# Optimization experiments

Measured on AMD Instinct MI355X. Metric: run time of the kernel, lower is better.

## Reference

```python
import jax, jax.numpy as jnp
import numpy as np

K = 8192      # codebook_dim
D = 256       # embedding_dim
BETA = 0.25
DECAY = 0.99
EPS = 1e-05


def setup_inputs() -> dict:
    key = jax.random.key(0)
    k1, k2, k3, k4 = jax.random.split(key, 4)
    lim = 1.0 / K
    return {
        "z": jax.random.normal(k1, (8, D, 32, 32), dtype=jnp.float32),
        "embedding": jax.random.uniform(k2, (K, D), minval=-lim, maxval=lim, dtype=jnp.float32),
        "cluster_size": jax.random.uniform(k3, (K,), dtype=jnp.float32),
        "ema_w": jax.random.uniform(k4, (K, D), minval=-lim, maxval=lim, dtype=jnp.float32),
    }


def reference(z, embedding, cluster_size, ema_w):
    # z: [B, C, H, W] -> [B, H, W, C]
    zp = jnp.transpose(z, (0, 2, 3, 1))
    zf = zp.reshape(-1, D)                                  # [N, D]
    # squared L2 distance to each code: ||z||^2 + ||e||^2 - 2 z.e
    d = (jnp.sum(zf * zf, axis=1, keepdims=True)
         + jnp.sum(embedding * embedding, axis=1)
         - 2.0 * jnp.einsum("nd,kd->nk", zf, embedding))    # [N, K]
    idx = jnp.argmin(d, axis=1)                             # [N]
    z_q = embedding[idx].reshape(zp.shape)                  # [B, H, W, C]

    # EMA update (training branch), expressed with segment sums instead of
    # materializing the one-hot [N, K] matrix.
    counts = jax.ops.segment_sum(jnp.ones_like(idx, dtype=zf.dtype), idx, num_segments=K)
    new_cs = cluster_size * DECAY + (1.0 - DECAY) * counts
    n = jnp.sum(new_cs)
    new_cs = (new_cs + EPS) / (n + K * EPS) * n
    dw = jax.ops.segment_sum(zf, idx, num_segments=K)       # encodings.T @ zf
    new_ema_w = ema_w * DECAY + (1.0 - DECAY) * dw
    new_embedding = new_ema_w / new_cs[:, None]

    sg = jax.lax.stop_gradient
    loss = jnp.mean((sg(z_q) - zp) ** 2) + BETA * jnp.mean((z_q - sg(zp)) ** 2)
    # straight-through estimator, back to NCHW
    z_q_out = jnp.transpose(zp + sg(z_q - zp), (0, 3, 1, 2))
    return z_q_out, loss, idx, new_cs, new_ema_w, new_embedding
```

## Files before the change

kernel.cpp:

```cpp
#include <hip/hip_runtime.h>

#define CHW 262144
#define HWD 1024

typedef _Float16 v8h __attribute__((ext_vector_type(8)));
typedef _Float16 v4h __attribute__((ext_vector_type(4)));
typedef float    v4f __attribute__((ext_vector_type(4)));

static const unsigned OFF_ASQ  = 0;
static const unsigned OFF_BSQ  = 8192;
static const unsigned OFF_CNT  = 16384;
static const unsigned OFF_HEAD = 24576;
static const unsigned OFF_NXT  = 32768;
static const unsigned OFF_SCAL = 40960;
static const unsigned OFF_AH   = 40968;
static const unsigned OFF_AM   = 1089544;
static const unsigned OFF_BH   = 2138120;
static const unsigned OFF_BM   = 3186696;

#define GLL(g, l) __builtin_amdgcn_global_load_lds( \
    (const __attribute__((address_space(1))) void*)(g), \
    (__attribute__((address_space(3))) void*)(l), 16, 0, 0)

__global__ __launch_bounds__(256) void k_prep(const float* __restrict__ z,
        const float* __restrict__ emb, float* __restrict__ asq, float* __restrict__ bsq,
        _Float16* __restrict__ Bh, _Float16* __restrict__ Bm,
        _Float16* __restrict__ Ah, _Float16* __restrict__ Am,
        float* __restrict__ zerobase) {
    int bx = blockIdx.x;
    int t = threadIdx.x;
    if (bx < 32) {
        int n = bx * 256 + t;
        const float* p = z + (size_t)(n >> 10) * CHW + (n & 1023);
        float s = 0.f;
        #pragma unroll 8
        for (int c = 0; c < 256; ++c) { float v = p[(size_t)c << 10]; s = fmaf(v, v, s); }
        asq[n] = s;
    } else if (bx < 2080) {
        int w = (bx - 32) * 4 + (t >> 6);
        int lane = t & 63;
        float4 v = *(const float4*)(emb + (size_t)w * 256 + lane * 4);
        float s = v.x * v.x;
        s = fmaf(v.y, v.y, s); s = fmaf(v.z, v.z, s); s = fmaf(v.w, v.w, s);
        #pragma unroll
        for (int m = 1; m < 64; m <<= 1) s += __shfl_xor(s, m, 64);
        if (lane == 0) bsq[w] = s;
        float e0 = v.x * 8192.0f, e1 = v.y * 8192.0f, e2 = v.z * 8192.0f, e3 = v.w * 8192.0f;
        _Float16 h0 = (_Float16)e0, h1 = (_Float16)e1, h2 = (_Float16)e2, h3 = (_Float16)e3;
        v4h hv = {h0, h1, h2, h3};
        v4h mv = {(_Float16)(e0 - (float)h0),
                  (_Float16)(e1 - (float)h1),
                  (_Float16)(e2 - (float)h2),
                  (_Float16)(e3 - (float)h3)};
        *(v4h*)(Bh + (size_t)w * 256 + lane * 4) = hv;
        *(v4h*)(Bm + (size_t)w * 256 + lane * 4) = mv;
    } else if (bx < 2592) {
        __shared__ float s[64][65];
        int blk = bx - 2080;
        int hw0 = (blk & 15) * 64;
        int c0  = ((blk >> 4) & 3) * 64;
        int b   = blk >> 6;
        #pragma unroll
        for (int ii = 0; ii < 16; ++ii) {
            int e = t + ii * 256;
            int c = e >> 6, x = e & 63;
            s[c][x] = z[(size_t)b * CHW + (size_t)(c0 + c) * HWD + hw0 + x];
        }
        __syncthreads();
        int n2 = t >> 2, cq = (t & 3) * 16;
        _Float16 hbuf[16], mbuf[16];
        #pragma unroll
        for (int j = 0; j < 16; ++j) {
            float v = s[cq + j][n2];
            _Float16 h = (_Float16)v;
            float r = v - (float)h;
            hbuf[j] = h;
            mbuf[j] = (_Float16)r;
        }
        size_t off = ((size_t)b * 1024 + hw0 + n2) * 256 + c0 + cq;
        *(v8h*)(Ah + off)     = *(v8h*)(hbuf);
        *(v8h*)(Ah + off + 8) = *(v8h*)(hbuf + 8);
        *(v8h*)(Am + off)     = *(v8h*)(mbuf);
        *(v8h*)(Am + off + 8) = *(v8h*)(mbuf + 8);
    } else {
        int idx = (bx - 2592) * 1024 + t * 4;
        *(float4*)(zerobase + idx) = (float4){0.f, 0.f, 0.f, 0.f};
        if (bx == 2592 && t == 0)
            *(float4*)(zerobase + 24576) = (float4){0.f, 0.f, 0.f, 0.f};
    }
}

__global__ __launch_bounds__(512, 2) void k_main(
        const _Float16* __restrict__ Ah, const _Float16* __restrict__ Am,
        const _Float16* __restrict__ Bh, const _Float16* __restrict__ Bm,
        const float* __restrict__ asq, const float* __restrict__ bsq,
        unsigned* __restrict__ pdk) {
    __shared__ _Float16 lds[65536];
    const int bid = blockIdx.x;
    const int xcd = bid & 7, sblk = bid >> 3;
    const int kt = xcd * 4 + (sblk & 3);
    const int nt = sblk >> 2;
    const int n0 = nt * 256, k0 = kt * 256;
    const int t = threadIdx.x;
    const int lane = t & 63, w = t >> 6;
    const int wrow = w >> 1, wcol = w & 1;
    const int lm = lane & 15, quad = lane >> 4;

    v4f acc[4][8];
    #pragma unroll
    for (int i = 0; i < 4; ++i)
        #pragma unroll
        for (int j = 0; j < 8; ++j) acc[i][j] = (v4f){0.f,0.f,0.f,0.f};

    const int row0 = t >> 2;
    const int c40 = (t & 3) ^ ((row0 >> 1) & 3);
    const char* gA  = (const char*)Ah + (size_t)(n0 + row0) * 512 + c40 * 16;
    const char* gAm = (const char*)Am + (size_t)(n0 + row0) * 512 + c40 * 16;
    const char* gB  = (const char*)Bh + (size_t)(k0 + row0) * 512 + c40 * 16;
    const char* gBm = (const char*)Bm + (size_t)(k0 + row0) * 512 + c40 * 16;

    int sa[4], sb[8];
    #pragma unroll
    for (int i = 0; i < 4; ++i) {
        int mr = wrow * 64 + i * 16 + lm;
        sa[i] = mr * 32 + ((quad ^ ((mr >> 1) & 3)) * 8);
    }
    #pragma unroll
    for (int j = 0; j < 8; ++j) {
        int nr = wcol * 128 + j * 16 + lm;
        sb[j] = nr * 32 + ((quad ^ ((nr >> 1) & 3)) * 8);
    }

    auto stageA = [&](int s) {
        const size_t co = (size_t)s * 64;
        _Float16* l = lds + (s & 1) * 32768 + t * 8;
        GLL(gA + co,          l);
        GLL(gA + co + 65536,  l + 4096);
    };
    auto stageB = [&](int s) {
        const size_t co = (size_t)s * 64;
        _Float16* l = lds + (s & 1) * 32768 + t * 8;
        GLL(gB + co,          l + 16384);
        GLL(gB + co + 65536,  l + 20480);
    };
    auto stageM = [&](int s) {
        const size_t co = (size_t)s * 64;
        _Float16* l = lds + (s & 1) * 32768 + t * 8;
        GLL(gAm + co,         l + 8192);
        GLL(gAm + co + 65536, l + 12288);
        GLL(gBm + co,         l + 24576);
        GLL(gBm + co + 65536, l + 28672);
    };

#define MFMA16(A, B, C) __builtin_amdgcn_mfma_f32_16x16x32_f16(A, B, C, 0, 0, 0)

    stageA(0); stageB(0); stageM(0);
    asm volatile("s_waitcnt vmcnt(4)" ::: "memory");
    __builtin_amdgcn_s_barrier();

    #pragma unroll
    for (int s = 0; s < 8; ++s) {
        const _Float16* L = lds + (s & 1) * 32768;

        v8h fa[4], fb[8];
        #pragma unroll
        for (int i = 0; i < 4; ++i) fa[i] = *(const v8h*)(L + sa[i]);
        #pragma unroll
        for (int j = 0; j < 8; ++j) fb[j] = *(const v8h*)(L + 16384 + sb[j]);
        if (s < 7) stageA(s + 1);
        __builtin_amdgcn_sched_barrier(0);
        __builtin_amdgcn_s_barrier();
        asm volatile("s_waitcnt lgkmcnt(0)" ::: "memory");
        __builtin_amdgcn_sched_barrier(0);
        __builtin_amdgcn_s_setprio(1);
        #pragma unroll
        for (int j = 0; j < 8; ++j)
            #pragma unroll
            for (int i = 0; i < 4; ++i)
                acc[i][j] = MFMA16(fa[i], fb[j], acc[i][j]);
        __builtin_amdgcn_s_setprio(0);
        __builtin_amdgcn_sched_barrier(0);
        if (s < 7) { asm volatile("s_waitcnt vmcnt(2)" ::: "memory"); }
        else       { asm volatile("s_waitcnt vmcnt(0)" ::: "memory"); }
        __builtin_amdgcn_s_barrier();

        v8h fbm[8];
        #pragma unroll
        for (int j = 0; j < 8; ++j) fbm[j] = *(const v8h*)(L + 24576 + sb[j]);
        if (s < 7) stageB(s + 1);
        __builtin_amdgcn_sched_barrier(0);
        __builtin_amdgcn_s_barrier();
        asm volatile("s_waitcnt lgkmcnt(0)" ::: "memory");
        __builtin_amdgcn_sched_barrier(0);
        __builtin_amdgcn_s_setprio(1);
        #pragma unroll
        for (int j = 0; j < 8; ++j)
            #pragma unroll
            for (int i = 0; i < 4; ++i)
                acc[i][j] = MFMA16(fa[i], fbm[j], acc[i][j]);
        __builtin_amdgcn_s_setprio(0);
        __builtin_amdgcn_sched_barrier(0);
        __builtin_amdgcn_s_barrier();

        v8h fam[4], fb2[8];
        #pragma unroll
        for (int i = 0; i < 4; ++i) fam[i] = *(const v8h*)(L + 8192 + sa[i]);
        #pragma unroll
        for (int j = 0; j < 8; ++j) fb2[j] = *(const v8h*)(L + 16384 + sb[j]);
        if (s < 7) stageM(s + 1);
        __builtin_amdgcn_sched_barrier(0);
        __builtin_amdgcn_s_barrier();
        asm volatile("s_waitcnt lgkmcnt(0)" ::: "memory");
        __builtin_amdgcn_sched_barrier(0);
        __builtin_amdgcn_s_setprio(1);
        #pragma unroll
        for (int j = 0; j < 8; ++j)
            #pragma unroll
            for (int i = 0; i < 4; ++i)
                acc[i][j] = MFMA16(fam[i], fb2[j], acc[i][j]);
        __builtin_amdgcn_s_setprio(0);
        __builtin_amdgcn_sched_barrier(0);
        if (s < 7) { asm volatile("s_waitcnt vmcnt(4)" ::: "memory"); }
        else       { asm volatile("s_waitcnt vmcnt(0)" ::: "memory"); }
        __builtin_amdgcn_s_barrier();
    }
#undef MFMA16

    float bvv[8];
    #pragma unroll
    for (int j = 0; j < 8; ++j) bvv[j] = bsq[k0 + wcol * 128 + j * 16 + lm];
    __syncthreads();
    unsigned* lrow = (unsigned*)lds;
    #pragma unroll
    for (int i = 0; i < 4; ++i) {
        #pragma unroll
        for (int r = 0; r < 4; ++r) {
            int mm = wrow * 64 + i * 16 + quad * 4 + r;
            float av_ = asq[n0 + mm];
            #pragma unroll
            for (int jh = 0; jh < 2; ++jh) {
                unsigned best = 0xFFFFFFFFu;
                #pragma unroll
                for (int j4 = 0; j4 < 4; ++j4) {
                    const int j = jh * 4 + j4;
                    float S = acc[i][j][r] * 1.220703125e-4f;
                    float dd = (av_ + bvv[j]) - 2.0f * S;
                    float gv = dd - av_;
                    int mi = (int)(gv * 65536.0f) + 32768;
                    int col = k0 + wcol * 128 + j * 16 + lm;
                    unsigned key = ((unsigned)mi << 13) | (unsigned)col;
                    best = key < best ? key : best;
                }
                #pragma unroll
                for (int xm = 1; xm < 16; xm <<= 1) {
                    unsigned o = __shfl_xor(best, xm, 64);
                    best = o < best ? o : best;
                }
                if (lm == 0)
                    lrow[(mm >> 7) * 512 + (wcol * 2 + jh) * 128 + (mm & 127)] = best;
            }
        }
    }
    __syncthreads();
    #pragma unroll
    for (int u = 0; u < 2; ++u) {
        int e = t + u * 512;
        pdk[((size_t)(nt * 2 + (e >> 9)) * 128 + kt * 4 + ((e >> 7) & 3)) * 128 + (e & 127)]
            = lrow[e];
    }
}

__global__ __launch_bounds__(256) void k_zqr(const unsigned* __restrict__ pdk,
        const float* __restrict__ z, const float* __restrict__ emb, const float* __restrict__ cs,
        float* __restrict__ out_idx, int* __restrict__ cnt,
        int* __restrict__ head, int* __restrict__ nxt,
        float* __restrict__ out_zq, float* __restrict__ scal) {
    const int bx = blockIdx.x, by = blockIdx.y;
    const int n0 = bx * 64, c00 = by * 64;
    const int lane = threadIdx.x & 63, g = threadIdx.x >> 6;
    const int nt = bx >> 1, mb = (bx & 1) * 64;

    unsigned mn = 0xFFFFFFFFu;
    const unsigned* base = pdk + (((size_t)nt * 128 + g * 32) << 7) + mb + lane;
    #pragma unroll 8
    for (int jj = 0; jj < 32; ++jj) {
        unsigned key = base[jj << 7];
        mn = key < mn ? key : mn;
    }
    __shared__ unsigned part[4][64];
    part[g][lane] = mn;
    __syncthreads();
    unsigned k0v = part[0][lane], k1v = part[1][lane];
    unsigned k2v = part[2][lane], k3v = part[3][lane];
    unsigned f01 = k0v < k1v ? k0v : k1v;
    unsigned f23 = k2v < k3v ? k2v : k3v;
    unsigned fkey = f01 < f23 ? f01 : f23;
    int idxn = (int)(fkey & 8191u);
    int n = n0 + lane;

    if (by == 0) {
        if (g == 0) {
            out_idx[n] = (float)idxn;
            atomicAdd(cnt + idxn, 1);
            int old = atomicExch(head + idxn, n + 1);
            nxt[n] = old;
        } else if (g == 1) {
            float cv = cs[n];
            #pragma unroll
            for (int m = 1; m < 64; m <<= 1) cv += __shfl_xor(cv, m, 64);
            if (lane == 0) atomicAdd(scal + 1, cv);
        }
    }

    int b = n >> 10, hw = n & 1023;
    const float* zr = z + (size_t)b * CHW + hw;
    const float* er = emb + (size_t)idxn * 256;
    float* oz = out_zq + (size_t)b * CHW + hw;
    float ls = 0.f;
    #pragma unroll
    for (int q = 0; q < 4; ++q) {
        int c = c00 + g * 16 + q * 4;
        float4 e4 = *(const float4*)(er + c);
        float ev[4] = {e4.x, e4.y, e4.z, e4.w};
        #pragma unroll
        for (int r = 0; r < 4; ++r) {
            float zp = zr[(size_t)(c + r) << 10];
            float dif = ev[r] - zp;
            oz[(size_t)(c + r) << 10] = zp + dif;
            ls = fmaf(dif, dif, ls);
        }
    }
    #pragma unroll
    for (int m = 1; m < 64; m <<= 1) ls += __shfl_xor(ls, m, 64);
    __shared__ float red[4];
    if (lane == 0) red[g] = ls;
    __syncthreads();
    if (threadIdx.x == 0) atomicAdd(scal, red[0] + red[1] + red[2] + red[3]);
}

__global__ __launch_bounds__(256) void k_fin(const float* __restrict__ cs, const float* __restrict__ ema,
        const int* __restrict__ head, const int* __restrict__ nxt,
        const _Float16* __restrict__ Ah, const _Float16* __restrict__ Am,
        const float* __restrict__ scal, const int* __restrict__ cnt,
        float* __restrict__ out_ncs, float* __restrict__ out_ema,
        float* __restrict__ out_emb, float* __restrict__ out_loss) {
    int k = blockIdx.x * 4 + (threadIdx.x >> 6);
    int lane = threadIdx.x & 63;
    float4 dwv = {0.f, 0.f, 0.f, 0.f};
    int cur = head[k];
    while (cur) {
        int n = cur - 1;
        v4h hh = *(const v4h*)(Ah + (size_t)n * 256 + lane * 4);
        v4h mm = *(const v4h*)(Am + (size_t)n * 256 + lane * 4);
        dwv.x += (float)hh[0] + (float)mm[0];
        dwv.y += (float)hh[1] + (float)mm[1];
        dwv.z += (float)hh[2] + (float)mm[2];
        dwv.w += (float)hh[3] + (float)mm[3];
        cur = nxt[n];
    }
    const float C1 = (float)(1.0 - 0.99);
    const float KEPS = (float)(8192 * 1e-5);
    float ncs0v = cs[k] * 0.99f + C1 * (float)cnt[k];
    float nsum = 0.99f * scal[1] + C1 * 8192.0f;
    float ncs = (ncs0v + 1e-5f) / (nsum + KEPS) * nsum;
    if (lane == 0) out_ncs[k] = ncs;
    size_t base = (size_t)k * 256 + lane * 4;
    float4 e4 = *(const float4*)(ema + base);
    float r0 = e4.x * 0.99f + C1 * dwv.x;
    float r1 = e4.y * 0.99f + C1 * dwv.y;
    float r2 = e4.z * 0.99f + C1 * dwv.z;
    float r3 = e4.w * 0.99f + C1 * dwv.w;
    out_ema[base + 0] = r0; out_ema[base + 1] = r1; out_ema[base + 2] = r2; out_ema[base + 3] = r3;
    out_emb[base + 0] = r0 / ncs; out_emb[base + 1] = r1 / ncs;
    out_emb[base + 2] = r2 / ncs; out_emb[base + 3] = r3 / ncs;
    if (blockIdx.x == 0 && threadIdx.x == 0) {
        float m = scal[0] * (1.0f / 2097152.0f);
        out_loss[0] = m + 0.25f * m;
    }
}

extern "C" void kernel_launch(void* const* d_in, const int* in_sizes, int n_in,
                              void* d_out, int out_size, void* d_ws, size_t ws_size,
                              hipStream_t stream) {
    const float* z   = (const float*)d_in[0];
    const float* emb = (const float*)d_in[1];
    const float* cs  = (const float*)d_in[2];
    const float* ema = (const float*)d_in[3];
    float* out = (float*)d_out;
    float* wsf = (float*)d_ws;

    float* asq  = wsf + OFF_ASQ;
    float* bsq  = wsf + OFF_BSQ;
    int*   cnt  = (int*)(wsf + OFF_CNT);
    int*   head = (int*)(wsf + OFF_HEAD);
    int*   nxt  = (int*)(wsf + OFF_NXT);
    float* scal = wsf + OFF_SCAL;
    _Float16* Ah = (_Float16*)(wsf + OFF_AH);
    _Float16* Am = (_Float16*)(wsf + OFF_AM);
    _Float16* Bh = (_Float16*)(wsf + OFF_BH);
    _Float16* Bm = (_Float16*)(wsf + OFF_BM);

    float* out_zq   = out;
    float* out_loss = out + 2097152;
    float* out_idx  = out + 2097153;
    float* out_ncs  = out + 2105345;
    float* out_ema  = out + 2113537;
    float* out_emb  = out + 4210689;

    unsigned* pdk = (unsigned*)(out + 2113540);

    k_prep<<<2608, 256, 0, stream>>>(z, emb, asq, bsq, Bh, Bm, Ah, Am, wsf + OFF_CNT);
    k_main<<<1024, 512, 0, stream>>>(Ah, Am, Bh, Bm, asq, bsq, pdk);
    k_zqr<<<dim3(128, 4), 256, 0, stream>>>(pdk, z, emb, cs, out_idx, cnt, head, nxt, out_zq, scal);
    k_fin<<<2048, 256, 0, stream>>>(cs, ema, head, nxt, Ah, Am, scal, cnt, out_ncs, out_ema, out_emb, out_loss);
}
```

Before: 222.4 us.

## Replace linked-list segment sum with atomic EMA accumulation and restructure main loop barriers

Drops the per-code linked-list gather in the finalize kernel. Instead, prep pre-scales ema_w by decay directly into the output, and the z_q kernel atomically adds C1*z into that row for each element. It also moves the barrier/wait points in the main MFMA loop so the next stage's global-to-LDS loads are issued before the fragment reads, and raises an unroll factor. Float atomics make the accumulation order nondeterministic, add contention on popular codes, and the pdk scratch area is relocated inside the output buffer.

```diff
diff --git a/kernel.cpp b/kernel.cpp
--- a/kernel.cpp
+++ b/kernel.cpp
@@ -10,8 +10,6 @@
 static const unsigned OFF_ASQ  = 0;
 static const unsigned OFF_BSQ  = 8192;
 static const unsigned OFF_CNT  = 16384;
-static const unsigned OFF_HEAD = 24576;
-static const unsigned OFF_NXT  = 32768;
 static const unsigned OFF_SCAL = 40960;
 static const unsigned OFF_AH   = 40968;
 static const unsigned OFF_AM   = 1089544;
@@ -26,14 +24,15 @@
         const float* __restrict__ emb, float* __restrict__ asq, float* __restrict__ bsq,
         _Float16* __restrict__ Bh, _Float16* __restrict__ Bm,
         _Float16* __restrict__ Ah, _Float16* __restrict__ Am,
-        float* __restrict__ zerobase) {
+        float* __restrict__ zerobase, const float* __restrict__ ema,
+        float* __restrict__ ema_acc) {
     int bx = blockIdx.x;
     int t = threadIdx.x;
     if (bx < 32) {
         int n = bx * 256 + t;
         const float* p = z + (size_t)(n >> 10) * CHW + (n & 1023);
         float s = 0.f;
-        #pragma unroll 8
+        #pragma unroll 32
         for (int c = 0; c < 256; ++c) { float v = p[(size_t)c << 10]; s = fmaf(v, v, s); }
         asq[n] = s;
     } else if (bx < 2080) {
@@ -82,11 +81,18 @@
         *(v8h*)(Ah + off + 8) = *(v8h*)(hbuf + 8);
         *(v8h*)(Am + off)     = *(v8h*)(mbuf);
         *(v8h*)(Am + off + 8) = *(v8h*)(mbuf + 8);
-    } else {
+    } else if (bx < 2600) {
         int idx = (bx - 2592) * 1024 + t * 4;
         *(float4*)(zerobase + idx) = (float4){0.f, 0.f, 0.f, 0.f};
         if (bx == 2592 && t == 0)
             *(float4*)(zerobase + 24576) = (float4){0.f, 0.f, 0.f, 0.f};
+    } else {
+        int i = (bx - 2600) * 1024 + t * 4;
+        float4 e = *(const float4*)(ema + i);
+        ema_acc[i + 0] = e.x * 0.99f;
+        ema_acc[i + 1] = e.y * 0.99f;
+        ema_acc[i + 2] = e.z * 0.99f;
+        ema_acc[i + 3] = e.w * 0.99f;
     }
 }
 
@@ -155,21 +161,20 @@
 #define MFMA16(A, B, C) __builtin_amdgcn_mfma_f32_16x16x32_f16(A, B, C, 0, 0, 0)
 
     stageA(0); stageB(0); stageM(0);
-    asm volatile("s_waitcnt vmcnt(4)" ::: "memory");
-    __builtin_amdgcn_s_barrier();
 
     #pragma unroll
     for (int s = 0; s < 8; ++s) {
         const _Float16* L = lds + (s & 1) * 32768;
 
+        asm volatile("s_waitcnt vmcnt(4)" ::: "memory");
+        __builtin_amdgcn_s_barrier();
+        __builtin_amdgcn_sched_barrier(0);
+        if (s < 7) stageA(s + 1);
         v8h fa[4], fb[8];
         #pragma unroll
         for (int i = 0; i < 4; ++i) fa[i] = *(const v8h*)(L + sa[i]);
         #pragma unroll
         for (int j = 0; j < 8; ++j) fb[j] = *(const v8h*)(L + 16384 + sb[j]);
-        if (s < 7) stageA(s + 1);
-        __builtin_amdgcn_sched_barrier(0);
-        __builtin_amdgcn_s_barrier();
         asm volatile("s_waitcnt lgkmcnt(0)" ::: "memory");
         __builtin_amdgcn_sched_barrier(0);
         __builtin_amdgcn_s_setprio(1);
@@ -180,16 +185,15 @@
                 acc[i][j] = MFMA16(fa[i], fb[j], acc[i][j]);
         __builtin_amdgcn_s_setprio(0);
         __builtin_amdgcn_sched_barrier(0);
+
         if (s < 7) { asm volatile("s_waitcnt vmcnt(2)" ::: "memory"); }
         else       { asm volatile("s_waitcnt vmcnt(0)" ::: "memory"); }
         __builtin_amdgcn_s_barrier();
-
+        __builtin_amdgcn_sched_barrier(0);
+        if (s < 7) stageB(s + 1);
         v8h fbm[8];
         #pragma unroll
         for (int j = 0; j < 8; ++j) fbm[j] = *(const v8h*)(L + 24576 + sb[j]);
-        if (s < 7) stageB(s + 1);
-        __builtin_amdgcn_sched_barrier(0);
-        __builtin_amdgcn_s_barrier();
         asm volatile("s_waitcnt lgkmcnt(0)" ::: "memory");
         __builtin_amdgcn_sched_barrier(0);
         __builtin_amdgcn_s_setprio(1);
@@ -200,16 +204,15 @@
                 acc[i][j] = MFMA16(fa[i], fbm[j], acc[i][j]);
         __builtin_amdgcn_s_setprio(0);
         __builtin_amdgcn_sched_barrier(0);
+
         __builtin_amdgcn_s_barrier();
-
+        __builtin_amdgcn_sched_barrier(0);
+        if (s < 7) stageM(s + 1);
         v8h fam[4], fb2[8];
         #pragma unroll
         for (int i = 0; i < 4; ++i) fam[i] = *(const v8h*)(L + 8192 + sa[i]);
         #pragma unroll
         for (int j = 0; j < 8; ++j) fb2[j] = *(const v8h*)(L + 16384 + sb[j]);
-        if (s < 7) stageM(s + 1);
-        __builtin_amdgcn_sched_barrier(0);
-        __builtin_amdgcn_s_barrier();
         asm volatile("s_waitcnt lgkmcnt(0)" ::: "memory");
         __builtin_amdgcn_sched_barrier(0);
         __builtin_amdgcn_s_setprio(1);
@@ -220,9 +223,6 @@
                 acc[i][j] = MFMA16(fam[i], fb2[j], acc[i][j]);
         __builtin_amdgcn_s_setprio(0);
         __builtin_amdgcn_sched_barrier(0);
-        if (s < 7) { asm volatile("s_waitcnt vmcnt(4)" ::: "memory"); }
-        else       { asm volatile("s_waitcnt vmcnt(0)" ::: "memory"); }
-        __builtin_amdgcn_s_barrier();
     }
 #undef MFMA16
 
@@ -273,8 +273,7 @@
 __global__ __launch_bounds__(256) void k_zqr(const unsigned* __restrict__ pdk,
         const float* __restrict__ z, const float* __restrict__ emb, const float* __restrict__ cs,
         float* __restrict__ out_idx, int* __restrict__ cnt,
-        int* __restrict__ head, int* __restrict__ nxt,
-        float* __restrict__ out_zq, float* __restrict__ scal) {
+        float* __restrict__ ema_acc, float* __restrict__ out_zq, float* __restrict__ scal) {
     const int bx = blockIdx.x, by = blockIdx.y;
     const int n0 = bx * 64, c00 = by * 64;
     const int lane = threadIdx.x & 63, g = threadIdx.x >> 6;
@@ -302,8 +301,6 @@
         if (g == 0) {
             out_idx[n] = (float)idxn;
             atomicAdd(cnt + idxn, 1);
-            int old = atomicExch(head + idxn, n + 1);
-            nxt[n] = old;
         } else if (g == 1) {
             float cv = cs[n];
             #pragma unroll
@@ -312,9 +309,11 @@
         }
     }
 
+    const float C1 = (float)(1.0 - 0.99);
     int b = n >> 10, hw = n & 1023;
     const float* zr = z + (size_t)b * CHW + hw;
     const float* er = emb + (size_t)idxn * 256;
+    float* ea = ema_acc + (size_t)idxn * 256;
     float* oz = out_zq + (size_t)b * CHW + hw;
     float ls = 0.f;
     #pragma unroll
@@ -328,6 +327,7 @@
             float dif = ev[r] - zp;
             oz[(size_t)(c + r) << 10] = zp + dif;
             ls = fmaf(dif, dif, ls);
+            atomicAdd(ea + c + r, C1 * zp);
         }
     }
     #pragma unroll
@@ -338,26 +338,12 @@
     if (threadIdx.x == 0) atomicAdd(scal, red[0] + red[1] + red[2] + red[3]);
 }
 
-__global__ __launch_bounds__(256) void k_fin(const float* __restrict__ cs, const float* __restrict__ ema,
-        const int* __restrict__ head, const int* __restrict__ nxt,
-        const _Float16* __restrict__ Ah, const _Float16* __restrict__ Am,
-        const float* __restrict__ scal, const int* __restrict__ cnt,
-        float* __restrict__ out_ncs, float* __restrict__ out_ema,
+__global__ __launch_bounds__(256) void k_fin(const float* __restrict__ cs,
+        const float* __restrict__ ema_acc, const float* __restrict__ scal,
+        const int* __restrict__ cnt, float* __restrict__ out_ncs,
         float* __restrict__ out_emb, float* __restrict__ out_loss) {
     int k = blockIdx.x * 4 + (threadIdx.x >> 6);
     int lane = threadIdx.x & 63;
-    float4 dwv = {0.f, 0.f, 0.f, 0.f};
-    int cur = head[k];
-    while (cur) {
-        int n = cur - 1;
-        v4h hh = *(const v4h*)(Ah + (size_t)n * 256 + lane * 4);
-        v4h mm = *(const v4h*)(Am + (size_t)n * 256 + lane * 4);
-        dwv.x += (float)hh[0] + (float)mm[0];
-        dwv.y += (float)hh[1] + (float)mm[1];
-        dwv.z += (float)hh[2] + (float)mm[2];
-        dwv.w += (float)hh[3] + (float)mm[3];
-        cur = nxt[n];
-    }
     const float C1 = (float)(1.0 - 0.99);
     const float KEPS = (float)(8192 * 1e-5);
     float ncs0v = cs[k] * 0.99f + C1 * (float)cnt[k];
@@ -365,12 +351,10 @@
     float ncs = (ncs0v + 1e-5f) / (nsum + KEPS) * nsum;
     if (lane == 0) out_ncs[k] = ncs;
     size_t base = (size_t)k * 256 + lane * 4;
-    float4 e4 = *(const float4*)(ema + base);
-    float r0 = e4.x * 0.99f + C1 * dwv.x;
-    float r1 = e4.y * 0.99f + C1 * dwv.y;
-    float r2 = e4.z * 0.99f + C1 * dwv.z;
-    float r3 = e4.w * 0.99f + C1 * dwv.w;
-    out_ema[base + 0] = r0; out_ema[base + 1] = r1; out_ema[base + 2] = r2; out_ema[base + 3] = r3;
+    float r0 = ema_acc[base + 0];
+    float r1 = ema_acc[base + 1];
+    float r2 = ema_acc[base + 2];
+    float r3 = ema_acc[base + 3];
     out_emb[base + 0] = r0 / ncs; out_emb[base + 1] = r1 / ncs;
     out_emb[base + 2] = r2 / ncs; out_emb[base + 3] = r3 / ncs;
     if (blockIdx.x == 0 && threadIdx.x == 0) {
@@ -392,8 +376,6 @@
     float* asq  = wsf + OFF_ASQ;
     float* bsq  = wsf + OFF_BSQ;
     int*   cnt  = (int*)(wsf + OFF_CNT);
-    int*   head = (int*)(wsf + OFF_HEAD);
-    int*   nxt  = (int*)(wsf + OFF_NXT);
     float* scal = wsf + OFF_SCAL;
     _Float16* Ah = (_Float16*)(wsf + OFF_AH);
     _Float16* Am = (_Float16*)(wsf + OFF_AM);
@@ -407,10 +389,12 @@
     float* out_ema  = out + 2113537;
     float* out_emb  = out + 4210689;
 
-    unsigned* pdk = (unsigned*)(out + 2113540);
-
-    k_prep<<<2608, 256, 0, stream>>>(z, emb, asq, bsq, Bh, Bm, Ah, Am, wsf + OFF_CNT);
+    unsigned* pdk = (unsigned*)(out + 4210692);
+
+    k_prep<<<4648, 256, 0, stream>>>(z, emb, asq, bsq, Bh, Bm, Ah, Am,
+                                     wsf + OFF_CNT, ema, out_ema);
     k_main<<<1024, 512, 0, stream>>>(Ah, Am, Bh, Bm, asq, bsq, pdk);
-    k_zqr<<<dim3(128, 4), 256, 0, stream>>>(pdk, z, emb, cs, out_idx, cnt, head, nxt, out_zq, scal);
-    k_fin<<<2048, 256, 0, stream>>>(cs, ema, head, nxt, Ah, Am, scal, cnt, out_ncs, out_ema, out_emb, out_loss);
+    k_zqr<<<dim3(128, 4), 256, 0, stream>>>(pdk, z, emb, cs, out_idx, cnt,
+                                            out_ema, out_zq, scal);
+    k_fin<<<2048, 256, 0, stream>>>(cs, out_ema, scal, cnt, out_ncs, out_emb, out_loss);
 }
```

Measured after the change: 318.8 us. 43.3% more time.
